# Optimization experiments

Measured on AMD Instinct MI355X. Metric: run time of the kernel, lower is better.

## Reference

```python
import jax, jax.numpy as jnp
import numpy as np

TEMPERATURE = 0.1
BASE_TEMPERATURE = 0.07
EPS = 1e-10


def setup_inputs() -> dict:
    key = jax.random.key(0)
    k1, k2 = jax.random.split(key)
    # feats_: [total_classes=64, n_view=128, feat_dim=256] sampled anchor features
    feats_ = jax.random.normal(k1, (64, 128, 256), dtype=jnp.float32)
    # labels_: class id per anchor group (21-class dataset -> repeats across groups)
    labels_ = jax.random.randint(k2, (64,), 0, 21, dtype=jnp.int32)
    return {"feats_": feats_, "labels_": labels_}


def reference(feats_, labels_):
    anchor_num, n_view, d = feats_.shape
    N = anchor_num * n_view
    # torch.cat(torch.unbind(feats_, dim=1), dim=0): view-major flattening
    cf = jnp.transpose(feats_, (1, 0, 2)).reshape(N, d)  # [N, d]
    # labels for the flattened ordering (mask.repeat tiles the [A,A] eq-mask)
    big_labels = jnp.tile(labels_, n_view)  # [N]

    logits = jnp.matmul(cf, cf.T) / TEMPERATURE  # [N, N]
    logits = logits - jax.lax.stop_gradient(jnp.max(logits, axis=1, keepdims=True))

    mask = (big_labels[:, None] == big_labels[None, :]).astype(jnp.float32)
    neg_mask = 1.0 - mask                       # negatives BEFORE removing diagonal
    mask = mask * (1.0 - jnp.eye(N, dtype=jnp.float32))  # positives exclude self

    exp_logits = jnp.exp(logits)
    neg_logits = jnp.sum(exp_logits * neg_mask, axis=1, keepdims=True)  # [N, 1]
    log_prob = logits - jnp.log(exp_logits + neg_logits + EPS)
    mean_log_prob_pos = jnp.sum(mask * log_prob, axis=1) / jnp.sum(mask, axis=1)
    loss = jnp.mean(-(TEMPERATURE / BASE_TEMPERATURE) * mean_log_prob_pos)
    return loss
```

## Files before the change

### kernel.cpp

```cpp
#include <hip/hip_runtime.h>
#include <hip/hip_bf16.h>

#define N_ROWS 8192
#define DIM 256
#define NANCH 64
#define NVIEW 128
#define NPART 8

typedef __attribute__((ext_vector_type(8))) short bf16x8;
typedef __attribute__((ext_vector_type(16))) float f32x16;
typedef __attribute__((ext_vector_type(4))) float float4v;
typedef __attribute__((ext_vector_type(4))) unsigned short ushort4v;

__device__ __forceinline__ unsigned short f2bf(float x) {
  union { float f; unsigned int u; } c; c.f = x;
  unsigned int u = c.u;
  unsigned int r = (u + 0x7fffu + ((u >> 16) & 1u)) >> 16;
  return (unsigned short)r;
}

__device__ __forceinline__ float bf2f(unsigned short b) {
  union { unsigned int u; float f; } c; c.u = ((unsigned int)b) << 16;
  return c.f;
}

__device__ __forceinline__ void gload_lds16(const void* g, void* l) {
  __builtin_amdgcn_global_load_lds(
      (const __attribute__((address_space(1))) unsigned int*)g,
      (__attribute__((address_space(3))) unsigned int*)l, 16, 0, 0);
}

__global__ void cast_diag_kernel(const float4v* __restrict__ in,
                                 ushort4v* __restrict__ out,
                                 float* __restrict__ diag) {
  const int w = threadIdx.x >> 6;
  const int l = threadIdx.x & 63;
  const int row = blockIdx.x * 4 + w;
  const float s = 3.16227766016838f;
  float4v v = in[row * 64 + l];
  ushort4v o;
  o.x = f2bf(v.x * s);
  o.y = f2bf(v.y * s);
  o.z = f2bf(v.z * s);
  o.w = f2bf(v.w * s);
  out[row * 64 + l] = o;
  float c0 = bf2f(o.x), c1 = bf2f(o.y), c2 = bf2f(o.z), c3 = bf2f(o.w);
  float ss = c0 * c0 + c1 * c1 + c2 * c2 + c3 * c3;
#pragma unroll
  for (int st = 1; st < 64; st <<= 1) ss += __shfl_xor(ss, st);
  if (l == 0) diag[row] = ss;
}

__global__ __launch_bounds__(256, 2) void pcl_negsum(
    const unsigned short* __restrict__ Xb, const int* __restrict__ labels,
    const float* __restrict__ diag, float* __restrict__ ns_partial,
    float* __restrict__ sd_partial, float* __restrict__ ep_partial) {
  const int bx = blockIdx.x;
  const int part = bx & 7;
  const int rb = bx >> 3;
  const int abase = part * 8;
  const int tid = threadIdx.x;
  const int wid = tid >> 6;
  const int lane = tid & 63;
  const int l31 = lane & 31;
  const int khalf = lane >> 5;
  const int rg = wid >> 1;
  const int cg = wid & 1;
  const int R0 = rb * 128;

  __shared__ __align__(16) unsigned short ring[2 * 64 * DIM];
  __shared__ float sdiag[128];
  __shared__ float nsacc[128];
  __shared__ float sdacc[128];
  __shared__ float epacc[128];
  __shared__ int slab[NANCH];

  if (tid < NANCH) slab[tid] = labels[tid];
  if (tid < 128) {
    sdiag[tid] = diag[R0 + tid];
    nsacc[tid] = 0.f;
    sdacc[tid] = 0.f;
    epacc[tid] = 0.f;
  }
  __syncthreads();
  const int myLab = slab[rb];

  bf16x8 afrag[2][16];
#pragma unroll
  for (int ri = 0; ri < 2; ++ri) {
#pragma unroll
    for (int ks = 0; ks < 16; ++ks) {
      const unsigned short* p =
          Xb + (size_t)(R0 + rg * 64 + ri * 32 + l31) * DIM + ks * 16 + khalf * 8;
      afrag[ri][ks] = *(const bf16x8*)p;
    }
  }
#pragma unroll
  for (int ri = 0; ri < 2; ++ri)
#pragma unroll
    for (int ks = 0; ks < 16; ++ks) asm volatile("" : "+v"(afrag[ri][ks]));

  float thr;
  {
    float d = sdiag[rg * 64 + lane];
#pragma unroll
    for (int st = 1; st < 64; st <<= 1) d = fminf(d, __shfl_xor(d, st));
    thr = d - 40.f;
  }

  char* const L0 = (char*)&ring[0];

#define STAGE(H)                                                                \
  do {                                                                          \
    const unsigned short* _s =                                                  \
        Xb + (size_t)((abase + ((H) >> 1)) * NVIEW + ((H) & 1) * 64 + lane) *   \
                 DIM + wid * 8;                                                 \
    char* _d = L0 + ((H) & 1) * 32768 + wid * 1024;                             \
    _Pragma("unroll") for (int i = 0; i < 8; ++i)                               \
        gload_lds16(_s + i * 32, _d + i * 4096);                                \
  } while (0)

  STAGE(0);

#define BODY(S, VNSTR)                                                          \
  do {                                                                          \
    if ((S) + 1 < 16) STAGE((S) + 1);                                           \
    asm volatile("s_waitcnt vmcnt(" VNSTR ")");                                 \
    __builtin_amdgcn_sched_barrier(0);                                          \
    __builtin_amdgcn_s_barrier();                                               \
    __builtin_amdgcn_sched_barrier(0);                                          \
    const char* _sb = L0 + ((S) & 1) * 32768 + khalf * 1024 + cg * 512 + l31 * 16; \
    f32x16 a0A = {}, a0B = {}, a1A = {}, a1B = {};                              \
    __builtin_amdgcn_s_setprio(1);                                              \
    _Pragma("unroll") for (int ks = 0; ks < 8; ++ks) {                          \
      bf16x8 b0 = *(const bf16x8*)(_sb + ks * 2048);                            \
      bf16x8 b1 = *(const bf16x8*)(_sb + (ks + 8) * 2048);                      \
      a0A = __builtin_amdgcn_mfma_f32_32x32x16_bf16(afrag[0][ks], b0, a0A, 0, 0, 0); \
      a1A = __builtin_amdgcn_mfma_f32_32x32x16_bf16(afrag[1][ks], b0, a1A, 0, 0, 0); \
      a0B = __builtin_amdgcn_mfma_f32_32x32x16_bf16(afrag[0][ks + 8], b1, a0B, 0, 0, 0); \
      a1B = __builtin_amdgcn_mfma_f32_32x32x16_bf16(afrag[1][ks + 8], b1, a1B, 0, 0, 0); \
    }                                                                           \
    __builtin_amdgcn_s_setprio(0);                                              \
    const bool is_pos = (slab[abase + ((S) >> 1)] == myLab);                    \
    f32x16 c0 = a0A + a0B;                                                      \
    f32x16 c1 = a1A + a1B;                                                      \
    float vmax = fmaxf(c0[0], c1[0]);                                           \
    _Pragma("unroll") for (int r = 1; r < 16; ++r)                              \
        vmax = fmaxf(vmax, fmaxf(c0[r], c1[r]));                                \
    const bool anyhot = __any(vmax > thr);                                      \
    if (__builtin_expect(is_pos, 0)) {                                          \
      if (!anyhot) {                                                            \
        _Pragma("unroll") for (int t2 = 0; t2 < 2; ++t2) {                      \
          _Pragma("unroll") for (int r = 0; r < 16; ++r) {                      \
            const int rloc = (r & 3) + 8 * (r >> 2) + 4 * khalf;                \
            const int row = rg * 64 + t2 * 32 + rloc;                           \
            float d = (t2 ? c1[r] : c0[r]) - sdiag[row];                        \
            _Pragma("unroll") for (int st = 1; st < 32; st <<= 1)               \
                d += __shfl_xor(d, st);                                         \
            if (l31 == 0) atomicAdd(&sdacc[row], d);                            \
          }                                                                     \
        }                                                                       \
      } else {                                                                  \
        const bool dt = (abase + ((S) >> 1)) == rb;                             \
        _Pragma("unroll") for (int t2 = 0; t2 < 2; ++t2) {                      \
          _Pragma("unroll") for (int r = 0; r < 16; ++r) {                      \
            const int rloc = (r & 3) + 8 * (r >> 2) + 4 * khalf;                \
            const int row = rg * 64 + t2 * 32 + rloc;                           \
            const int cl = ((S) & 1) * 64 + cg * 32 + l31;                      \
            const bool isdiag = dt && (row == cl);                              \
            float v = (t2 ? c1[r] : c0[r]);                                     \
            float d = v - sdiag[row];                                           \
            float sd_e = isdiag ? 0.f : d;                                      \
            float e = (!isdiag && d > -40.f) ? __expf(d) : 0.f;                 \
            _Pragma("unroll") for (int st = 1; st < 32; st <<= 1) {             \
              sd_e += __shfl_xor(sd_e, st);                                     \
              e += __shfl_xor(e, st);                                           \
            }                                                                   \
            if (l31 == 0) {                                                     \
              atomicAdd(&sdacc[row], sd_e);                                     \
              if (e != 0.f) atomicAdd(&epacc[row], e);                          \
            }                                                                   \
          }                                                                     \
        }                                                                       \
      }                                                                         \
    } else if (__builtin_expect(anyhot, 0)) {                                   \
      _Pragma("unroll") for (int t2 = 0; t2 < 2; ++t2) {                        \
        _Pragma("unroll") for (int r = 0; r < 16; ++r) {                        \
          const int rloc = (r & 3) + 8 * (r >> 2) + 4 * khalf;                  \
          const int row = rg * 64 + t2 * 32 + rloc;                             \
          float d = (t2 ? c1[r] : c0[r]) - sdiag[row];                          \
          float e = (d > -40.f) ? __expf(d) : 0.f;                              \
          _Pragma("unroll") for (int st = 1; st < 32; st <<= 1)                 \
              e += __shfl_xor(e, st);                                           \
          if (l31 == 0) atomicAdd(&nsacc[row], e);                              \
        }                                                                       \
      }                                                                         \
    }                                                                           \
    __builtin_amdgcn_s_barrier();                                               \
  } while (0)

  BODY(0, "8");  BODY(1, "8");  BODY(2, "8");  BODY(3, "8");
  BODY(4, "8");  BODY(5, "8");  BODY(6, "8");  BODY(7, "8");
  BODY(8, "8");  BODY(9, "8");  BODY(10, "8"); BODY(11, "8");
  BODY(12, "8"); BODY(13, "8"); BODY(14, "8"); BODY(15, "0");

#undef BODY
#undef STAGE

  __syncthreads();
  if (tid < 128) {
    ns_partial[part * N_ROWS + R0 + tid] = nsacc[tid];
    sd_partial[part * N_ROWS + R0 + tid] = sdacc[tid];
    ep_partial[part * N_ROWS + R0 + tid] = epacc[tid];
  }
}

__global__ void pcl_combine(const int* __restrict__ labels,
                            const float* __restrict__ ns_partial,
                            const float* __restrict__ sd_partial,
                            const float* __restrict__ ep_partial,
                            float* __restrict__ partials) {
  const int tid = threadIdx.x;
  const int row = blockIdx.x * 256 + tid;
  __shared__ int slab[NANCH];
  __shared__ float sred[256];
  if (tid < NANCH) slab[tid] = labels[tid];
  __syncthreads();

  const int lab = slab[row >> 7];
  int cnt = 0;
#pragma unroll
  for (int b = 0; b < NANCH; ++b) cnt += (slab[b] == lab) ? 1 : 0;

  float NS = 0.f, SD = 0.f, EP = 0.f;
#pragma unroll
  for (int p = 0; p < NPART; ++p) {
    NS += ns_partial[p * N_ROWS + row];
    SD += sd_partial[p * N_ROWS + row];
    EP += ep_partial[p * N_ROWS + row];
  }
  const float npos = (float)(cnt * NVIEW - 1);
  const float nse = NS + 1e-10f;
  const float mlpp = (SD - npos * __logf(nse) - EP / nse) / npos;
  sred[tid] = mlpp;
  __syncthreads();
  for (int st = 128; st > 0; st >>= 1) {
    if (tid < st) sred[tid] += sred[tid + st];
    __syncthreads();
  }
  if (tid == 0) partials[blockIdx.x] = sred[0];
}

__global__ void final_reduce(const float* __restrict__ partials, float* __restrict__ out) {
  __shared__ float s[32];
  int t = threadIdx.x;
  if (t < 32) s[t] = partials[t];
  __syncthreads();
  if (t == 0) {
    float sum = 0.f;
    for (int r = 0; r < 32; ++r) sum += s[r];
    out[0] = -(0.1f / 0.07f) * sum / (float)N_ROWS;
  }
}

extern "C" void kernel_launch(void* const* d_in, const int* in_sizes, int n_in,
                              void* d_out, int out_size, void* d_ws, size_t ws_size,
                              hipStream_t stream) {
  const float* feats = (const float*)d_in[0];
  const int* labels = (const int*)d_in[1];
  float* out = (float*)d_out;

  char* base = (char*)d_ws;
  unsigned short* Xb = (unsigned short*)d_ws;
  size_t off = (size_t)N_ROWS * DIM * 2;
  float* diag = (float*)(base + off);       off += N_ROWS * 4;
  float* ns_partial = (float*)(base + off); off += NPART * N_ROWS * 4;
  float* sd_partial = (float*)(base + off); off += NPART * N_ROWS * 4;
  float* ep_partial = (float*)(base + off); off += NPART * N_ROWS * 4;
  float* partials = (float*)(base + off);

  cast_diag_kernel<<<N_ROWS / 4, 256, 0, stream>>>((const float4v*)feats,
                                                   (ushort4v*)Xb, diag);
  pcl_negsum<<<NANCH * NPART, 256, 0, stream>>>(Xb, labels, diag, ns_partial,
                                                sd_partial, ep_partial);
  pcl_combine<<<N_ROWS / 256, 256, 0, stream>>>(labels, ns_partial, sd_partial,
                                                ep_partial, partials);
  final_reduce<<<1, 64, 0, stream>>>(partials, out);
}
```

Before: 93.78 us.

## Retile negsum kernel to 256-row blocks with triple-buffered 32-column stages

Each block now owns 256 rows, one 64-row slab per wave instead of a 2x2 wave grid, and splits the columns into 16 partitions of 4 anchors. The LDS ring changes from two 64-column buffers to three 32-column buffers, prefetching two stages ahead. The aim is to cut redundant B-tile loads per row and hide more load latency. The trade-off is half as many blocks (512 to 512 still, but a different row/column split), a larger partial-sum array for the combine kernel, and each wave now computing a 64x32 tile per stage. The combine kernel must also read NPART=16 partials, and its hidden code is assumed to be driven by that macro.

```diff
diff --git a/kernel.cpp b/kernel.cpp
--- a/kernel.cpp
+++ b/kernel.cpp
@@ -5,7 +5,7 @@
 #define DIM 256
 #define NANCH 64
 #define NVIEW 128
-#define NPART 8
+#define NPART 16
 
 typedef __attribute__((ext_vector_type(8))) short bf16x8;
 typedef __attribute__((ext_vector_type(16))) float f32x16;
@@ -56,34 +56,33 @@
     const float* __restrict__ diag, float* __restrict__ ns_partial,
     float* __restrict__ sd_partial, float* __restrict__ ep_partial) {
   const int bx = blockIdx.x;
-  const int part = bx & 7;
-  const int rb = bx >> 3;
-  const int abase = part * 8;
+  const int rb = bx & 31;
+  const int part = bx >> 5;
+  const int abase = part * 4;
   const int tid = threadIdx.x;
   const int wid = tid >> 6;
   const int lane = tid & 63;
   const int l31 = lane & 31;
   const int khalf = lane >> 5;
-  const int rg = wid >> 1;
-  const int cg = wid & 1;
-  const int R0 = rb * 128;
-
-  __shared__ __align__(16) unsigned short ring[2 * 64 * DIM];
-  __shared__ float sdiag[128];
-  __shared__ float nsacc[128];
-  __shared__ float sdacc[128];
-  __shared__ float epacc[128];
+  const int R0 = rb * 256;
+
+  __shared__ __align__(16) unsigned short ring[3 * 32 * DIM];
+  __shared__ float sdiag[256];
+  __shared__ float nsacc[256];
+  __shared__ float sdacc[256];
+  __shared__ float epacc[256];
   __shared__ int slab[NANCH];
 
   if (tid < NANCH) slab[tid] = labels[tid];
-  if (tid < 128) {
+  if (tid < 256) {
     sdiag[tid] = diag[R0 + tid];
     nsacc[tid] = 0.f;
     sdacc[tid] = 0.f;
     epacc[tid] = 0.f;
   }
   __syncthreads();
-  const int myLab = slab[rb];
+  const int myAnch = rb * 2 + (wid >> 1);
+  const int myLab = slab[myAnch];
 
   bf16x8 afrag[2][16];
 #pragma unroll
@@ -91,7 +90,7 @@
 #pragma unroll
     for (int ks = 0; ks < 16; ++ks) {
       const unsigned short* p =
-          Xb + (size_t)(R0 + rg * 64 + ri * 32 + l31) * DIM + ks * 16 + khalf * 8;
+          Xb + (size_t)(R0 + wid * 64 + ri * 32 + l31) * DIM + ks * 16 + khalf * 8;
       afrag[ri][ks] = *(const bf16x8*)p;
     }
   }
@@ -102,7 +101,7 @@
 
   float thr;
   {
-    float d = sdiag[rg * 64 + lane];
+    float d = sdiag[wid * 64 + lane];
 #pragma unroll
     for (int st = 1; st < 64; st <<= 1) d = fminf(d, __shfl_xor(d, st));
     thr = d - 40.f;
@@ -112,36 +111,39 @@
 
 #define STAGE(H)                                                                \
   do {                                                                          \
+    const int _cb = (abase + ((H) >> 2)) * NVIEW + ((H) & 3) * 32;              \
     const unsigned short* _s =                                                  \
-        Xb + (size_t)((abase + ((H) >> 1)) * NVIEW + ((H) & 1) * 64 + lane) *   \
-                 DIM + wid * 8;                                                 \
-    char* _d = L0 + ((H) & 1) * 32768 + wid * 1024;                             \
-    _Pragma("unroll") for (int i = 0; i < 8; ++i)                               \
-        gload_lds16(_s + i * 32, _d + i * 4096);                                \
+        Xb + (size_t)(_cb + l31) * DIM + (wid * 2 + khalf) * 8;                 \
+    char* _d = L0 + ((H) % 3) * 16384 + wid * 1024;                             \
+    gload_lds16(_s, _d);                                                        \
+    gload_lds16(_s + 64, _d + 4096);                                            \
+    gload_lds16(_s + 128, _d + 8192);                                           \
+    gload_lds16(_s + 192, _d + 12288);                                          \
   } while (0)
 
   STAGE(0);
+  STAGE(1);
 
 #define BODY(S, VNSTR)                                                          \
   do {                                                                          \
-    if ((S) + 1 < 16) STAGE((S) + 1);                                           \
+    if ((S) + 2 < 16) STAGE((S) + 2);                                           \
     asm volatile("s_waitcnt vmcnt(" VNSTR ")");                                 \
     __builtin_amdgcn_sched_barrier(0);                                          \
     __builtin_amdgcn_s_barrier();                                               \
     __builtin_amdgcn_sched_barrier(0);                                          \
-    const char* _sb = L0 + ((S) & 1) * 32768 + khalf * 1024 + cg * 512 + l31 * 16; \
+    const char* _sb = L0 + ((S) % 3) * 16384 + khalf * 512 + l31 * 16;          \
     f32x16 a0A = {}, a0B = {}, a1A = {}, a1B = {};                              \
     __builtin_amdgcn_s_setprio(1);                                              \
     _Pragma("unroll") for (int ks = 0; ks < 8; ++ks) {                          \
-      bf16x8 b0 = *(const bf16x8*)(_sb + ks * 2048);                            \
-      bf16x8 b1 = *(const bf16x8*)(_sb + (ks + 8) * 2048);                      \
+      bf16x8 b0 = *(const bf16x8*)(_sb + ks * 1024);                            \
+      bf16x8 b1 = *(const bf16x8*)(_sb + (ks + 8) * 1024);                      \
       a0A = __builtin_amdgcn_mfma_f32_32x32x16_bf16(afrag[0][ks], b0, a0A, 0, 0, 0); \
       a1A = __builtin_amdgcn_mfma_f32_32x32x16_bf16(afrag[1][ks], b0, a1A, 0, 0, 0); \
       a0B = __builtin_amdgcn_mfma_f32_32x32x16_bf16(afrag[0][ks + 8], b1, a0B, 0, 0, 0); \
       a1B = __builtin_amdgcn_mfma_f32_32x32x16_bf16(afrag[1][ks + 8], b1, a1B, 0, 0, 0); \
     }                                                                           \
     __builtin_amdgcn_s_setprio(0);                                              \
-    const bool is_pos = (slab[abase + ((S) >> 1)] == myLab);                    \
+    const bool is_pos = (slab[abase + ((S) >> 2)] == myLab);                    \
     f32x16 c0 = a0A + a0B;                                                      \
     f32x16 c1 = a1A + a1B;                                                      \
     float vmax = fmaxf(c0[0], c1[0]);                                           \
@@ -153,7 +155,7 @@
         _Pragma("unroll") for (int t2 = 0; t2 < 2; ++t2) {                      \
           _Pragma("unroll") for (int r = 0; r < 16; ++r) {                      \
             const int rloc = (r & 3) + 8 * (r >> 2) + 4 * khalf;                \
-            const int row = rg * 64 + t2 * 32 + rloc;                           \
+            const int row = wid * 64 + t2 * 32 + rloc;                          \
             float d = (t2 ? c1[r] : c0[r]) - sdiag[row];                        \
             _Pragma("unroll") for (int st = 1; st < 32; st <<= 1)               \
                 d += __shfl_xor(d, st);                                         \
@@ -161,13 +163,14 @@
           }                                                                     \
         }                                                                       \
       } else {                                                                  \
-        const bool dt = (abase + ((S) >> 1)) == rb;                             \
+        const bool dt = (abase + ((S) >> 2)) == myAnch;                         \
         _Pragma("unroll") for (int t2 = 0; t2 < 2; ++t2) {                      \
           _Pragma("unroll") for (int r = 0; r < 16; ++r) {                      \
             const int rloc = (r & 3) + 8 * (r >> 2) + 4 * khalf;                \
-            const int row = rg * 64 + t2 * 32 + rloc;                           \
-            const int cl = ((S) & 1) * 64 + cg * 32 + l31;                      \
-            const bool isdiag = dt && (row == cl);                              \
+            const int row = wid * 64 + t2 * 32 + rloc;                          \
+            const bool isdiag =                                                 \
+                dt && (((wid & 1) * 64 + t2 * 32 + rloc) ==                     \
+                       (((S) & 3) * 32 + l31));                                 \
             float v = (t2 ? c1[r] : c0[r]);                                     \
             float d = v - sdiag[row];                                           \
             float sd_e = isdiag ? 0.f : d;                                      \
@@ -187,7 +190,7 @@
       _Pragma("unroll") for (int t2 = 0; t2 < 2; ++t2) {                        \
         _Pragma("unroll") for (int r = 0; r < 16; ++r) {                        \
           const int rloc = (r & 3) + 8 * (r >> 2) + 4 * khalf;                  \
-          const int row = rg * 64 + t2 * 32 + rloc;                             \
+          const int row = wid * 64 + t2 * 32 + rloc;                            \
           float d = (t2 ? c1[r] : c0[r]) - sdiag[row];                          \
           float e = (d > -40.f) ? __expf(d) : 0.f;                              \
           _Pragma("unroll") for (int st = 1; st < 32; st <<= 1)                 \
@@ -202,13 +205,13 @@
   BODY(0, "8");  BODY(1, "8");  BODY(2, "8");  BODY(3, "8");
   BODY(4, "8");  BODY(5, "8");  BODY(6, "8");  BODY(7, "8");
   BODY(8, "8");  BODY(9, "8");  BODY(10, "8"); BODY(11, "8");
-  BODY(12, "8"); BODY(13, "8"); BODY(14, "8"); BODY(15, "0");
+  BODY(12, "8"); BODY(13, "8"); BODY(14, "4"); BODY(15, "0");
 
 #undef BODY
 #undef STAGE
 
   __syncthreads();
-  if (tid < 128) {
+  if (tid < 256) {
     ns_partial[part * N_ROWS + R0 + tid] = nsacc[tid];
     sd_partial[part * N_ROWS + R0 + tid] = sdacc[tid];
     ep_partial[part * N_ROWS + R0 + tid] = epacc[tid];
@@ -274,15 +277,15 @@
   unsigned short* Xb = (unsigned short*)d_ws;
   size_t off = (size_t)N_ROWS * DIM * 2;
   float* diag = (float*)(base + off);       off += N_ROWS * 4;
-  float* ns_partial = (float*)(base + off); off += NPART * N_ROWS * 4;
-  float* sd_partial = (float*)(base + off); off += NPART * N_ROWS * 4;
-  float* ep_partial = (float*)(base + off); off += NPART * N_ROWS * 4;
+  float* ns_partial = (float*)(base + off); off += (size_t)NPART * N_ROWS * 4;
+  float* sd_partial = (float*)(base + off); off += (size_t)NPART * N_ROWS * 4;
+  float* ep_partial = (float*)(base + off); off += (size_t)NPART * N_ROWS * 4;
   float* partials = (float*)(base + off);
 
   cast_diag_kernel<<<N_ROWS / 4, 256, 0, stream>>>((const float4v*)feats,
                                                    (ushort4v*)Xb, diag);
-  pcl_negsum<<<NANCH * NPART, 256, 0, stream>>>(Xb, labels, diag, ns_partial,
-                                                sd_partial, ep_partial);
+  pcl_negsum<<<32 * NPART, 256, 0, stream>>>(Xb, labels, diag, ns_partial,
+                                             sd_partial, ep_partial);
   pcl_combine<<<N_ROWS / 256, 256, 0, stream>>>(labels, ns_partial, sd_partial,
                                                 ep_partial, partials);
   final_reduce<<<1, 64, 0, stream>>>(partials, out);
```

New measurement: 133.6 us. 1.42x slower.
